# Performance work log

Hardware: AMD Instinct MI355X
Metric: run time of the kernel (lower is better)

The kernel has to match this reference:

```python
import jax, jax.numpy as jnp
import numpy as np

N_NODES = 50000
N_EDGES = 500000
H_DIM = 128
OUT_DIM = 16
N_RELS = 90
N_BASES = 4


def setup_inputs() -> dict:
    key = jax.random.key(0)
    ks = jax.random.split(key, 12)
    inp = {
        'node_ids': jnp.arange(N_NODES, dtype=jnp.int32),
        'src': jax.random.randint(ks[0], (N_EDGES,), 0, N_NODES, dtype=jnp.int32),
        'dst': jax.random.randint(ks[1], (N_EDGES,), 0, N_NODES, dtype=jnp.int32),
        'etype': jax.random.randint(ks[2], (N_EDGES,), 0, N_RELS, dtype=jnp.int32),
        'emb': jax.random.normal(ks[3], (N_NODES, H_DIM), jnp.float32),
        'basis1': jax.random.normal(ks[4], (N_BASES, H_DIM, H_DIM), jnp.float32) * (1.0 / np.sqrt(H_DIM)),
        'comp1': jax.random.normal(ks[5], (N_RELS, N_BASES), jnp.float32) * (1.0 / np.sqrt(N_BASES)),
        'loop_w1': jax.random.normal(ks[6], (H_DIM, H_DIM), jnp.float32) * (1.0 / np.sqrt(H_DIM)),
        'bias1': jnp.zeros((H_DIM,), jnp.float32),
        'basis2': jax.random.normal(ks[7], (N_BASES, H_DIM, OUT_DIM), jnp.float32) * (1.0 / np.sqrt(H_DIM)),
        'comp2': jax.random.normal(ks[8], (N_RELS, N_BASES), jnp.float32) * (1.0 / np.sqrt(N_BASES)),
        'loop_w2': jax.random.normal(ks[9], (H_DIM, OUT_DIM), jnp.float32) * (1.0 / np.sqrt(H_DIM)),
        'bias2': jnp.zeros((OUT_DIM,), jnp.float32),
    }
    return inp


def _rel_graph_conv(x, src, dst, etype, basis, comp, loop_w, bias, num_nodes):
    # Basis decomposition: W_r = sum_b comp[r,b] * basis[b].
    # Project node features through each basis first (N is smaller than E),
    # then combine per-edge with relation coefficients: avoids per-edge GEMM.
    xb = jnp.einsum('ni,bio->nbo', x, basis)            # [N, B, out]
    msg = jnp.einsum('eb,ebo->eo', comp[etype], xb[src])  # [E, out]
    agg = jax.ops.segment_sum(msg, dst, num_segments=num_nodes)  # [N, out]
    # apply_norm=True: divide aggregated messages by in-degree of dst.
    deg = jax.ops.segment_sum(jnp.ones((src.shape[0],), x.dtype), dst,
                              num_segments=num_nodes)
    h = agg * (1.0 / jnp.maximum(deg, 1.0))[:, None]
    # self_loop=True plus bias.
    return h + x @ loop_w + bias


def reference(node_ids, src, dst, etype, emb, basis1, comp1, loop_w1, bias1,
              basis2, comp2, loop_w2, bias2):
    n = emb.shape[0]
    x = emb[node_ids]                                   # embedding lookup
    h = jax.nn.relu(_rel_graph_conv(x, src, dst, etype, basis1, comp1,
                                    loop_w1, bias1, n))
    out = _rel_graph_conv(h, src, dst, etype, basis2, comp2, loop_w2, bias2, n)
    return out
```

## Files before the change

kernel.cpp:

```cpp
#include <hip/hip_runtime.h>
#include <hip/hip_bf16.h>

#define N_NODES 50000
#define N_EDGES 500000
#define H_DIM 128
#define OUT_DIM 16
#define KDIM 640

typedef short short8 __attribute__((ext_vector_type(8)));
typedef float f32x4 __attribute__((ext_vector_type(4)));
typedef float f32x2 __attribute__((ext_vector_type(2)));

__device__ inline unsigned short f2b(float f) {
  unsigned u = __float_as_uint(f);
  u += 0x7fffu + ((u >> 16) & 1u);
  return (unsigned short)(u >> 16);
}
__device__ inline float b2f(unsigned short u) {
  return __uint_as_float(((unsigned)u) << 16);
}

#define CONV_BLOCKS 6250
#define PREP_BLOCKS 360
#define INIT_BLOCKS 196
__global__ void prologue_kernel(const int* __restrict__ node_ids, const float* __restrict__ emb,
                                unsigned short* __restrict__ Abuf,
                                const float* __restrict__ basis1, const float* __restrict__ loop_w1,
                                const float* __restrict__ basis2, const float* __restrict__ loop_w2,
                                unsigned short* __restrict__ B1t, unsigned short* __restrict__ B2pt,
                                int* __restrict__ cntA, int* __restrict__ cntB,
                                int* __restrict__ counter) {
  int b = blockIdx.x;
  if (b < CONV_BLOCKS) {
    int tid = b * 256 + threadIdx.x;
    if (tid >= N_NODES * (H_DIM / 4)) return;
    int n = tid >> 5;
    int q = tid & 31;
    int id = node_ids[n];
    const float4 v = *reinterpret_cast<const float4*>(emb + (size_t)id * H_DIM + q * 4);
    uint2 p;
    p.x = (unsigned)f2b(v.x) | ((unsigned)f2b(v.y) << 16);
    p.y = (unsigned)f2b(v.z) | ((unsigned)f2b(v.w) << 16);
    *reinterpret_cast<uint2*>(Abuf + (size_t)n * KDIM + 512 + q * 4) = p;
  } else if (b < CONV_BLOCKS + PREP_BLOCKS) {
    int tid = (b - CONV_BLOCKS) * 256 + threadIdx.x;
    if (tid < 128 * KDIM) {
      int c = tid / KDIM, k = tid % KDIM;
      float v = (k < 512) ? basis1[k * 128 + c] : loop_w1[(k - 512) * 128 + c];
      B1t[c * KDIM + k] = f2b(v);
    } else if (tid < 128 * KDIM + 80 * 128) {
      int t2 = tid - 128 * KDIM;
      int c = t2 / 128, k = t2 % 128;
      float v = (c < 64) ? basis2[(c >> 4) * 128 * 16 + k * 16 + (c & 15)]
                         : loop_w2[k * 16 + (c - 64)];
      B2pt[c * 128 + k] = f2b(v);
    }
  } else {
    int i = (b - CONV_BLOCKS - PREP_BLOCKS) * 256 + threadIdx.x;
    if (i < N_NODES) {
      cntA[i] = 0;
      cntB[i] = 0;
    }
    if (i == 0) *counter = 0;
  }
}

__global__ void count_kernel(const int* __restrict__ dst, int* __restrict__ cnt) {
  for (int e = blockIdx.x * blockDim.x + threadIdx.x; e < N_EDGES; e += gridDim.x * blockDim.x)
    atomicAdd(&cnt[dst[e]], 1);
}

__global__ void alloc_kernel(const int* __restrict__ cnt, int* __restrict__ start,
                             int* __restrict__ counter) {
  int i = blockIdx.x * blockDim.x + threadIdx.x;
  int lane = threadIdx.x & 63;
  int c = (i < N_NODES) ? cnt[i] : 0;
  int incl = c;
#pragma unroll
  for (int off = 1; off < 64; off <<= 1) {
    int v = __shfl_up(incl, off, 64);
    if (lane >= off) incl += v;
  }
  int waveTotal = __shfl(incl, 63, 64);
  int base = 0;
  if (lane == 63) base = atomicAdd(counter, waveTotal);
  base = __shfl(base, 63, 64);
  if (i < N_NODES) start[i] = base + incl - c;
}

__global__ void fill_kernel(const int* __restrict__ src, const int* __restrict__ dst,
                            const int* __restrict__ et, const int* __restrict__ csr_start,
                            int* __restrict__ cnt, int2* __restrict__ csr_se) {
  for (int e = blockIdx.x * blockDim.x + threadIdx.x; e < N_EDGES; e += gridDim.x * blockDim.x) {
    int d = dst[e];
    int idx = csr_start[d] + atomicAdd(&cnt[d], 1);
    csr_se[idx] = make_int2(src[e], et[e]);
  }
}

__global__ __launch_bounds__(256) void agg_kernel(const int* __restrict__ csr_start,
                                                  const int* __restrict__ csr_cnt,
                                                  const int2* __restrict__ csr_se,
                                                  const float* __restrict__ comp,
                                                  unsigned short* __restrict__ Abuf) {
  int node = blockIdx.x * 4 + (threadIdx.x >> 6);
  if (node >= N_NODES) return;
  int lane = threadIdx.x & 63;
  int lo = __builtin_amdgcn_readfirstlane(csr_start[node]);
  int deg = __builtin_amdgcn_readfirstlane(csr_cnt[node]);
  int hi = lo + deg;

  f32x2 a0 = {0.f, 0.f}, a1 = {0.f, 0.f}, a2 = {0.f, 0.f}, a3 = {0.f, 0.f};
  const unsigned short* featb = Abuf + 512;
  const int laneoff = lane * 2;

#define EDGE_BODY(J)                                                                   \
  {                                                                                    \
    int s = __builtin_amdgcn_readlane(myse.x, (J));                                    \
    int t = __builtin_amdgcn_readlane(myse.y, (J));                                    \
    unsigned u = *reinterpret_cast<const unsigned*>(featb + s * KDIM + laneoff);       \
    float4 c = *reinterpret_cast<const float4*>(comp + t * 4);                         \
    f32x2 x;                                                                           \
    x.x = __uint_as_float(u << 16);                                                    \
    x.y = __uint_as_float(u & 0xffff0000u);                                            \
    a0 = __builtin_elementwise_fma((f32x2){c.x, c.x}, x, a0);                          \
    a1 = __builtin_elementwise_fma((f32x2){c.y, c.y}, x, a1);                          \
    a2 = __builtin_elementwise_fma((f32x2){c.z, c.z}, x, a2);                          \
    a3 = __builtin_elementwise_fma((f32x2){c.w, c.w}, x, a3);                          \
  }

  for (int e0 = lo; e0 < hi; e0 += 64) {
    int nchunk = min(hi - e0, 64);
    int2 myse = make_int2(0, 0);
    if (e0 + lane < hi) myse = csr_se[e0 + lane];
    int j = 0;
    for (; j + 4 <= nchunk; j += 4) {
      EDGE_BODY(j)
      EDGE_BODY(j + 1)
      EDGE_BODY(j + 2)
      EDGE_BODY(j + 3)
    }
    for (; j < nchunk; ++j) { EDGE_BODY(j) }
  }
#undef EDGE_BODY

  float inv = 1.0f / (float)(deg > 0 ? deg : 1);
  unsigned short* out = Abuf + (size_t)node * KDIM;
  unsigned p0w = (unsigned)f2b(a0.x * inv) | ((unsigned)f2b(a0.y * inv) << 16);
  unsigned p1w = (unsigned)f2b(a1.x * inv) | ((unsigned)f2b(a1.y * inv) << 16);
  unsigned p2w = (unsigned)f2b(a2.x * inv) | ((unsigned)f2b(a2.y * inv) << 16);
  unsigned p3w = (unsigned)f2b(a3.x * inv) | ((unsigned)f2b(a3.y * inv) << 16);
  *reinterpret_cast<unsigned*>(out + 0 * 128 + laneoff) = p0w;
  *reinterpret_cast<unsigned*>(out + 1 * 128 + laneoff) = p1w;
  *reinterpret_cast<unsigned*>(out + 2 * 128 + laneoff) = p2w;
  *reinterpret_cast<unsigned*>(out + 3 * 128 + laneoff) = p3w;
}

__global__ __launch_bounds__(256) void agg2_kernel(const int* __restrict__ csr_start,
                                                   const int* __restrict__ csr_cnt,
                                                   const int2* __restrict__ csr_se,
                                                   const float* __restrict__ comp,
                                                   const unsigned short* __restrict__ Abuf,
                                                   const float* __restrict__ bias2,
                                                   float* __restrict__ dout) {
  int node = blockIdx.x * 4 + (threadIdx.x >> 6);
  if (node >= N_NODES) return;
  int lane = threadIdx.x & 63;
  int bsel = lane >> 4;
  int o = lane & 15;
  int lo = __builtin_amdgcn_readfirstlane(csr_start[node]);
  int deg = __builtin_amdgcn_readfirstlane(csr_cnt[node]);
  int hi = lo + deg;

  float acc = 0.f;

#define EDGE2_BODY(J)                                                      \
  {                                                                        \
    int s = __builtin_amdgcn_readlane(myse.x, (J));                        \
    int t = __builtin_amdgcn_readlane(myse.y, (J));                        \
    unsigned short u = Abuf[s * KDIM + lane];                              \
    float4 c = *reinterpret_cast<const float4*>(comp + t * 4);             \
    float cb = (bsel < 2) ? ((bsel == 0) ? c.x : c.y)                      \
                          : ((bsel == 2) ? c.z : c.w);                     \
    acc = fmaf(cb, b2f(u), acc);                                           \
  }

  for (int e0 = lo; e0 < hi; e0 += 64) {
    int nchunk = min(hi - e0, 64);
    int2 myse = make_int2(0, 0);
    if (e0 + lane < hi) myse = csr_se[e0 + lane];
    int j = 0;
    for (; j + 4 <= nchunk; j += 4) {
      EDGE2_BODY(j)
      EDGE2_BODY(j + 1)
      EDGE2_BODY(j + 2)
      EDGE2_BODY(j + 3)
    }
    for (; j < nchunk; ++j) { EDGE2_BODY(j) }
  }
#undef EDGE2_BODY

  acc += __shfl_xor(acc, 16, 64);
  acc += __shfl_xor(acc, 32, 64);

  if (lane < 16) {
    float inv = 1.0f / (float)(deg > 0 ? deg : 1);
    float sl = b2f(Abuf[(size_t)node * KDIM + 64 + o]);
    dout[(size_t)node * OUT_DIM + o] = acc * inv + sl + bias2[o];
  }
}

template <int BM, int NC, int KT, bool RELU, bool HAS_BIAS>
__global__ __launch_bounds__(256) void gemm_kernel(const unsigned short* __restrict__ A,
                                                   int a_stride,
                                                   const unsigned short* __restrict__ Bt,
                                                   int bt_stride,
                                                   const float* __restrict__ bias,
                                                   unsigned short* __restrict__ outp,
                                                   int out_stride, int M) {
  constexpr int RT = BM / 64;
  __shared__ unsigned short As[BM][64];
  __shared__ unsigned short Bs[NC][64];
  int wave = threadIdx.x >> 6;
  int lane = threadIdx.x & 63;
  int row0 = blockIdx.x * BM;
  f32x4 acc[RT][NC / 16] = {};

  int kh = lane >> 4;
  int cl = lane & 15;

  for (int k0 = 0; k0 < KT; k0 += 64) {
#pragma unroll
    for (int p = 0; p < BM * 8 / 256; ++p) {
      int cid = threadIdx.x + p * 256;
      int r = cid >> 3, c8 = cid & 7;
      int gr = row0 + r;
      short8 v = {};
      if (gr < M) v = *reinterpret_cast<const short8*>(A + (size_t)gr * a_stride + k0 + c8 * 8);
      *reinterpret_cast<short8*>(&As[r][(c8 ^ (r & 7)) * 8]) = v;
    }
    for (int cid = threadIdx.x; cid < NC * 8; cid += 256) {
      int r = cid >> 3, c8 = cid & 7;
      short8 v = *reinterpret_cast<const short8*>(Bt + (size_t)r * bt_stride + k0 + c8 * 8);
      *reinterpret_cast<short8*>(&Bs[r][(c8 ^ (r & 7)) * 8]) = v;
    }
    __syncthreads();
    short8 af[RT][2];
#pragma unroll
    for (int rt = 0; rt < RT; ++rt) {
      int ar = wave * (16 * RT) + rt * 16 + cl;
      af[rt][0] = *reinterpret_cast<const short8*>(&As[ar][((kh) ^ (ar & 7)) * 8]);
      af[rt][1] = *reinterpret_cast<const short8*>(&As[ar][((4 + kh) ^ (ar & 7)) * 8]);
    }
#pragma unroll
    for (int ct = 0; ct < NC / 16; ++ct) {
      int bc = ct * 16 + cl;
      short8 b0 = *reinterpret_cast<const short8*>(&Bs[bc][((kh) ^ (bc & 7)) * 8]);
      short8 b1 = *reinterpret_cast<const short8*>(&Bs[bc][((4 + kh) ^ (bc & 7)) * 8]);
#pragma unroll
      for (int rt = 0; rt < RT; ++rt) {
        acc[rt][ct] = __builtin_amdgcn_mfma_f32_16x16x32_bf16(af[rt][0], b0, acc[rt][ct], 0, 0, 0);
        acc[rt][ct] = __builtin_amdgcn_mfma_f32_16x16x32_bf16(af[rt][1], b1, acc[rt][ct], 0, 0, 0);
      }
    }
    __syncthreads();
  }
#pragma unroll
  for (int rt = 0; rt < RT; ++rt) {
    int rb = row0 + wave * (16 * RT) + rt * 16 + (lane >> 4) * 4;
#pragma unroll
    for (int ct = 0; ct < NC / 16; ++ct) {
      int col = ct * 16 + cl;
      float bv = HAS_BIAS ? bias[col] : 0.f;
#pragma unroll
      for (int r = 0; r < 4; ++r) {
        int gr = rb + r;
        if (gr < M) {
          float v = acc[rt][ct][r] + bv;
          if (RELU) v = fmaxf(v, 0.0f);
          outp[(size_t)gr * out_stride + col] = f2b(v);
        }
      }
    }
  }
}

extern "C" void kernel_launch(void* const* d_in, const int* in_sizes, int n_in,
                              void* d_out, int out_size, void* d_ws, size_t ws_size,
                              hipStream_t stream) {
  const int* node_ids = (const int*)d_in[0];
  const int* src = (const int*)d_in[1];
  const int* dst = (const int*)d_in[2];
  const int* etype = (const int*)d_in[3];
  const float* emb = (const float*)d_in[4];
  const float* basis1 = (const float*)d_in[5];
  const float* comp1 = (const float*)d_in[6];
  const float* loop_w1 = (const float*)d_in[7];
  const float* bias1 = (const float*)d_in[8];
  const float* basis2 = (const float*)d_in[9];
  const float* comp2 = (const float*)d_in[10];
  const float* loop_w2 = (const float*)d_in[11];
  const float* bias2 = (const float*)d_in[12];
  (void)in_sizes; (void)n_in; (void)out_size; (void)ws_size;

  char* ws = (char*)d_ws;
  size_t off = 0;
  auto alloc = [&](size_t bytes) -> void* {
    void* p = ws + off;
    off += (bytes + 255) & ~(size_t)255;
    return p;
  };
  int* csr_start = (int*)alloc(N_NODES * sizeof(int));
  int* cntA = (int*)alloc(N_NODES * sizeof(int));
  int* cntB = (int*)alloc(N_NODES * sizeof(int));
  int* counter = (int*)alloc(sizeof(int));
  int2* csr_se = (int2*)alloc((size_t)N_EDGES * sizeof(int2));
  unsigned short* Abuf = (unsigned short*)alloc((size_t)N_NODES * KDIM * sizeof(unsigned short));
  unsigned short* B1t = (unsigned short*)alloc(128 * KDIM * sizeof(unsigned short));
  unsigned short* B2pt = (unsigned short*)alloc(80 * 128 * sizeof(unsigned short));

  prologue_kernel<<<CONV_BLOCKS + PREP_BLOCKS + INIT_BLOCKS, 256, 0, stream>>>(
      node_ids, emb, Abuf, basis1, loop_w1, basis2, loop_w2, B1t, B2pt, cntA, cntB, counter);
  count_kernel<<<1024, 256, 0, stream>>>(dst, cntA);
  alloc_kernel<<<(N_NODES + 255) / 256, 256, 0, stream>>>(cntA, csr_start, counter);
  fill_kernel<<<1024, 256, 0, stream>>>(src, dst, etype, csr_start, cntB, csr_se);

  agg_kernel<<<(N_NODES + 3) / 4, 256, 0, stream>>>(csr_start, cntA, csr_se, comp1, Abuf);
  gemm_kernel<128, 128, KDIM, true, true><<<(N_NODES + 127) / 128, 256, 0, stream>>>(
      Abuf, KDIM, B1t, KDIM, bias1, Abuf + 512, KDIM, N_NODES);

  gemm_kernel<64, 80, 128, false, false><<<(N_NODES + 63) / 64, 256, 0, stream>>>(
      Abuf + 512, KDIM, B2pt, 128, nullptr, Abuf, KDIM, N_NODES);
  agg2_kernel<<<(N_NODES + 3) / 4, 256, 0, stream>>>(csr_start, cntA, csr_se, comp2, Abuf,
                                                     bias2, (float*)d_out);
}
```

Measured before the change: 176.4 us.

## Fuse layer-1 GEMM with layer-2 projection GEMM via shared-memory hidden tile

Merges the two GEMM launches into one kernel. Each block computes a 64-row tile of the layer-1 output with bias and ReLU, keeps it in LDS as bf16, and multiplies it directly by the layer-2 basis/loop weights. This removes one launch and the global re-read of the hidden activations. In exchange the layer-1 tile shrinks from 128 to 64 rows, so B1 is reloaded by twice as many blocks, and LDS use grows, which may lower occupancy.

```diff
diff --git a/kernel.cpp b/kernel.cpp
--- a/kernel.cpp
+++ b/kernel.cpp
@@ -210,77 +210,105 @@
   }
 }
 
-template <int BM, int NC, int KT, bool RELU, bool HAS_BIAS>
-__global__ __launch_bounds__(256) void gemm_kernel(const unsigned short* __restrict__ A,
-                                                   int a_stride,
-                                                   const unsigned short* __restrict__ Bt,
-                                                   int bt_stride,
-                                                   const float* __restrict__ bias,
-                                                   unsigned short* __restrict__ outp,
-                                                   int out_stride, int M) {
-  constexpr int RT = BM / 64;
-  __shared__ unsigned short As[BM][64];
-  __shared__ unsigned short Bs[NC][64];
+__global__ __launch_bounds__(256) void gemm1p_kernel(const unsigned short* __restrict__ A,
+                                                     const unsigned short* __restrict__ B1t,
+                                                     const float* __restrict__ bias1,
+                                                     const unsigned short* __restrict__ B2pt,
+                                                     unsigned short* __restrict__ Abuf, int M) {
+  __shared__ unsigned short As[64][64];
+  __shared__ unsigned short Bs[128][64];
+  __shared__ unsigned short Hs[64][128];
   int wave = threadIdx.x >> 6;
   int lane = threadIdx.x & 63;
-  int row0 = blockIdx.x * BM;
-  f32x4 acc[RT][NC / 16] = {};
-
+  int row0 = blockIdx.x * 64;
   int kh = lane >> 4;
   int cl = lane & 15;
-
-  for (int k0 = 0; k0 < KT; k0 += 64) {
-#pragma unroll
-    for (int p = 0; p < BM * 8 / 256; ++p) {
+  int ar = wave * 16 + cl;
+  f32x4 acc[8] = {};
+
+  for (int k0 = 0; k0 < KDIM; k0 += 64) {
+#pragma unroll
+    for (int p = 0; p < 2; ++p) {
       int cid = threadIdx.x + p * 256;
       int r = cid >> 3, c8 = cid & 7;
       int gr = row0 + r;
       short8 v = {};
-      if (gr < M) v = *reinterpret_cast<const short8*>(A + (size_t)gr * a_stride + k0 + c8 * 8);
+      if (gr < M) v = *reinterpret_cast<const short8*>(A + (size_t)gr * KDIM + k0 + c8 * 8);
       *reinterpret_cast<short8*>(&As[r][(c8 ^ (r & 7)) * 8]) = v;
     }
-    for (int cid = threadIdx.x; cid < NC * 8; cid += 256) {
+#pragma unroll
+    for (int p = 0; p < 4; ++p) {
+      int cid = threadIdx.x + p * 256;
       int r = cid >> 3, c8 = cid & 7;
-      short8 v = *reinterpret_cast<const short8*>(Bt + (size_t)r * bt_stride + k0 + c8 * 8);
+      short8 v = *reinterpret_cast<const short8*>(B1t + (size_t)r * KDIM + k0 + c8 * 8);
       *reinterpret_cast<short8*>(&Bs[r][(c8 ^ (r & 7)) * 8]) = v;
     }
     __syncthreads();
-    short8 af[RT][2];
-#pragma unroll
-    for (int rt = 0; rt < RT; ++rt) {
-      int ar = wave * (16 * RT) + rt * 16 + cl;
-      af[rt][0] = *reinterpret_cast<const short8*>(&As[ar][((kh) ^ (ar & 7)) * 8]);
-      af[rt][1] = *reinterpret_cast<const short8*>(&As[ar][((4 + kh) ^ (ar & 7)) * 8]);
-    }
-#pragma unroll
-    for (int ct = 0; ct < NC / 16; ++ct) {
+    short8 a0 = *reinterpret_cast<const short8*>(&As[ar][((kh) ^ (ar & 7)) * 8]);
+    short8 a1 = *reinterpret_cast<const short8*>(&As[ar][((4 + kh) ^ (ar & 7)) * 8]);
+#pragma unroll
+    for (int ct = 0; ct < 8; ++ct) {
       int bc = ct * 16 + cl;
       short8 b0 = *reinterpret_cast<const short8*>(&Bs[bc][((kh) ^ (bc & 7)) * 8]);
       short8 b1 = *reinterpret_cast<const short8*>(&Bs[bc][((4 + kh) ^ (bc & 7)) * 8]);
-#pragma unroll
-      for (int rt = 0; rt < RT; ++rt) {
-        acc[rt][ct] = __builtin_amdgcn_mfma_f32_16x16x32_bf16(af[rt][0], b0, acc[rt][ct], 0, 0, 0);
-        acc[rt][ct] = __builtin_amdgcn_mfma_f32_16x16x32_bf16(af[rt][1], b1, acc[rt][ct], 0, 0, 0);
-      }
+      acc[ct] = __builtin_amdgcn_mfma_f32_16x16x32_bf16(a0, b0, acc[ct], 0, 0, 0);
+      acc[ct] = __builtin_amdgcn_mfma_f32_16x16x32_bf16(a1, b1, acc[ct], 0, 0, 0);
     }
     __syncthreads();
   }
-#pragma unroll
-  for (int rt = 0; rt < RT; ++rt) {
-    int rb = row0 + wave * (16 * RT) + rt * 16 + (lane >> 4) * 4;
-#pragma unroll
-    for (int ct = 0; ct < NC / 16; ++ct) {
-      int col = ct * 16 + cl;
-      float bv = HAS_BIAS ? bias[col] : 0.f;
-#pragma unroll
-      for (int r = 0; r < 4; ++r) {
-        int gr = rb + r;
-        if (gr < M) {
-          float v = acc[rt][ct][r] + bv;
-          if (RELU) v = fmaxf(v, 0.0f);
-          outp[(size_t)gr * out_stride + col] = f2b(v);
-        }
-      }
+
+  int rb = wave * 16 + (lane >> 4) * 4;
+#pragma unroll
+  for (int ct = 0; ct < 8; ++ct) {
+    int col = ct * 16 + cl;
+    float bv = bias1[col];
+#pragma unroll
+    for (int r = 0; r < 4; ++r) {
+      int lr = rb + r;
+      int gr = row0 + lr;
+      float v = fmaxf(acc[ct][r] + bv, 0.0f);
+      unsigned short hb = f2b(v);
+      if (gr < M) Abuf[(size_t)gr * KDIM + 512 + col] = hb;
+      int c8 = col >> 3;
+      int c8s = (c8 & 8) | ((c8 ^ lr) & 7);
+      *reinterpret_cast<unsigned short*>(
+          reinterpret_cast<char*>(&Hs[lr][0]) + c8s * 16 + (col & 7) * 2) = hb;
+    }
+  }
+  __syncthreads();
+
+  f32x4 acc2[5] = {};
+  for (int k0 = 0; k0 < 128; k0 += 64) {
+    for (int cid = threadIdx.x; cid < 80 * 8; cid += 256) {
+      int r = cid >> 3, c8 = cid & 7;
+      short8 v = *reinterpret_cast<const short8*>(B2pt + r * 128 + k0 + c8 * 8);
+      *reinterpret_cast<short8*>(&Bs[r][(c8 ^ (r & 7)) * 8]) = v;
+    }
+    __syncthreads();
+    int c8a = (k0 >> 3) + kh;
+    int c8b = (k0 >> 3) + 4 + kh;
+    short8 a0 = *reinterpret_cast<const short8*>(
+        reinterpret_cast<char*>(&Hs[ar][0]) + (((c8a ^ ar) & 7) | (c8a & 8)) * 16);
+    short8 a1 = *reinterpret_cast<const short8*>(
+        reinterpret_cast<char*>(&Hs[ar][0]) + (((c8b ^ ar) & 7) | (c8b & 8)) * 16);
+#pragma unroll
+    for (int ct = 0; ct < 5; ++ct) {
+      int bc = ct * 16 + cl;
+      short8 b0 = *reinterpret_cast<const short8*>(&Bs[bc][((kh) ^ (bc & 7)) * 8]);
+      short8 b1 = *reinterpret_cast<const short8*>(&Bs[bc][((4 + kh) ^ (bc & 7)) * 8]);
+      acc2[ct] = __builtin_amdgcn_mfma_f32_16x16x32_bf16(a0, b0, acc2[ct], 0, 0, 0);
+      acc2[ct] = __builtin_amdgcn_mfma_f32_16x16x32_bf16(a1, b1, acc2[ct], 0, 0, 0);
+    }
+    __syncthreads();
+  }
+
+#pragma unroll
+  for (int ct = 0; ct < 5; ++ct) {
+    int col = ct * 16 + cl;
+#pragma unroll
+    for (int r = 0; r < 4; ++r) {
+      int gr = row0 + rb + r;
+      if (gr < M) Abuf[(size_t)gr * KDIM + col] = f2b(acc2[ct][r]);
     }
   }
 }
@@ -326,11 +354,8 @@
   fill_kernel<<<1024, 256, 0, stream>>>(src, dst, etype, csr_start, cntB, csr_se);
 
   agg_kernel<<<(N_NODES + 3) / 4, 256, 0, stream>>>(csr_start, cntA, csr_se, comp1, Abuf);
-  gemm_kernel<128, 128, KDIM, true, true><<<(N_NODES + 127) / 128, 256, 0, stream>>>(
-      Abuf, KDIM, B1t, KDIM, bias1, Abuf + 512, KDIM, N_NODES);
-
-  gemm_kernel<64, 80, 128, false, false><<<(N_NODES + 63) / 64, 256, 0, stream>>>(
-      Abuf + 512, KDIM, B2pt, 128, nullptr, Abuf, KDIM, N_NODES);
+  gemm1p_kernel<<<(N_NODES + 63) / 64, 256, 0, stream>>>(Abuf, B1t, bias1, B2pt, Abuf, N_NODES);
+
   agg2_kernel<<<(N_NODES + 3) / 4, 256, 0, stream>>>(csr_start, cntA, csr_se, comp2, Abuf,
                                                      bias2, (float*)d_out);
 }
```

Result: faster. 154.9 us (-12.2%).
